# Kernel optimization log

Measured on AMD Instinct MI355X. Metric: run time of the kernel, lower is better.

## Reference

```python
import jax, jax.numpy as jnp
import numpy as np
from jax import lax

B, L, D = 4, 4096, 1024
EXPAND, K = 2, 4
INNER = D * EXPAND  # 2048


def setup_inputs() -> dict:
    key = jax.random.key(0)
    k0, k1, k2, k3, k4 = jax.random.split(key, 5)
    s = 0.02
    return {
        "x": jax.random.normal(k0, (B, L, D), jnp.float32),
        "W_in": jax.random.normal(k1, (D, 2 * INNER), jnp.float32) * s,
        "conv_w": jax.random.normal(k2, (INNER, 1, K), jnp.float32) * s,  # depthwise [out, in/groups=1, k]
        "conv_b": jax.random.normal(k3, (INNER,), jnp.float32) * s,
        "W_out": jax.random.normal(k4, (INNER, D), jnp.float32) * s,
    }


def reference(x, W_in, conv_w, conv_b, W_out):
    # Linear (no bias): [B,L,D] -> [B,L,2*INNER]
    h = jnp.einsum("bld,df->blf", x, W_in)
    # GLU(dim=-1): first half gated by sigmoid of second half
    a, g = jnp.split(h, 2, axis=-1)
    h = a * jax.nn.sigmoid(g)  # [B,L,INNER]
    # depthwise causal Conv1d: torch pads both sides by K-1 then slices [:, :, :L],
    # which equals left-padding by K-1 only.
    hc = jnp.transpose(h, (0, 2, 1))  # [B,INNER,L]
    y = lax.conv_general_dilated(
        hc, conv_w,
        window_strides=(1,),
        padding=[(K - 1, 0)],
        dimension_numbers=("NCH", "OIH", "NCH"),
        feature_group_count=INNER,
    ) + conv_b[None, :, None]  # [B,INNER,L]
    y = jax.nn.silu(y)
    y = jnp.transpose(y, (0, 2, 1))  # [B,L,INNER]
    # Output linear (no bias): [B,L,INNER] -> [B,L,D]
    return jnp.einsum("blf,fd->bld", y, W_out)
```

## Files before the change

kernel.cpp:

```cpp
#include <hip/hip_runtime.h>
#include <hip/hip_bf16.h>

constexpr int B_ = 4, L_ = 4096, D_ = 1024, INNER_ = 2048;
constexpr int M_ = B_ * L_;
constexpr int N1_ = 2 * INNER_;

typedef __attribute__((ext_vector_type(4))) float f32x4;
typedef __attribute__((ext_vector_type(8))) short short8;

#define DEV static __device__ __forceinline__

DEV short f2bfs(float f) {
  __hip_bfloat16 h = __float2bfloat16(f);
  return __builtin_bit_cast(short, h);
}
DEV float bfs2f(short s) {
  unsigned int u = ((unsigned int)(unsigned short)s) << 16;
  return __builtin_bit_cast(float, u);
}

DEV void gload_lds16(const void* g, void* l) {
  __builtin_amdgcn_global_load_lds(
      (const __attribute__((address_space(1))) unsigned int*)g,
      (__attribute__((address_space(3))) unsigned int*)l,
      16, 0, 0);
}

__global__ void k_cvt(const float4* __restrict__ in, short4* __restrict__ out, int n4) {
  int i = blockIdx.x * blockDim.x + threadIdx.x;
  if (i >= n4) return;
  float4 v = in[i];
  short4 o;
  o.x = f2bfs(v.x); o.y = f2bfs(v.y); o.z = f2bfs(v.z); o.w = f2bfs(v.w);
  out[i] = o;
}

__global__ void k_transpose_cvt(const float* __restrict__ W, short* __restrict__ Wt,
                                int R, int C) {
  __shared__ short tile[32][33];
  int tx = threadIdx.x & 31;
  int ty = threadIdx.x >> 5;
  int c0 = blockIdx.x * 32;
  int r0 = blockIdx.y * 32;
#pragma unroll
  for (int i = 0; i < 32; i += 8)
    tile[ty + i][tx] = f2bfs(W[(size_t)(r0 + ty + i) * C + (c0 + tx)]);
  __syncthreads();
#pragma unroll
  for (int i = 0; i < 32; i += 8)
    Wt[(size_t)(c0 + ty + i) * R + (r0 + tx)] = tile[tx][ty + i];
}

__global__ __launch_bounds__(256, 2) void k_gemm1_glu(
    const short* __restrict__ A, const short* __restrict__ Bt,
    short* __restrict__ G) {
  constexpr int K = 1024, BK = 32, NK = K / BK;
  __shared__ short sA[128 * 32];
  __shared__ short sBa[128 * 32];
  __shared__ short sBg[128 * 32];

  const int tid = threadIdx.x;
  const int wid = tid >> 6;
  const int lane = tid & 63;
  const int m0 = blockIdx.x * 128;
  const int n0 = blockIdx.y * 128;

  const int srow = wid * 32 + (lane >> 2);
  const int scol = (lane & 3) * 8;

  const int wr = wid >> 1, wc = wid & 1;
  const int l16 = lane & 15, kg = lane >> 4;

  const f32x4 vzero = {0.f, 0.f, 0.f, 0.f};
  f32x4 acc_a[4][4], acc_g[4][4];
#pragma unroll
  for (int m = 0; m < 4; ++m)
#pragma unroll
    for (int n = 0; n < 4; ++n) { acc_a[m][n] = vzero; acc_g[m][n] = vzero; }

  for (int kt = 0; kt < NK; ++kt) {
    const int k0 = kt * BK;
#pragma unroll
    for (int j = 0; j < 2; ++j) {
      const int r = srow + j * 16;
      gload_lds16(A + (size_t)(m0 + r) * K + k0 + scol, &sA[(wid * 32 + j * 16) * 32]);
      gload_lds16(Bt + (size_t)(n0 + r) * K + k0 + scol, &sBa[(wid * 32 + j * 16) * 32]);
      gload_lds16(Bt + (size_t)(n0 + 2048 + r) * K + k0 + scol, &sBg[(wid * 32 + j * 16) * 32]);
    }
    __syncthreads();

    short8 af[4], ba[4], bg[4];
#pragma unroll
    for (int m = 0; m < 4; ++m)
      af[m] = *(const short8*)&sA[(wr * 64 + m * 16 + l16) * 32 + kg * 8];
#pragma unroll
    for (int n = 0; n < 4; ++n) {
      ba[n] = *(const short8*)&sBa[(wc * 64 + n * 16 + l16) * 32 + kg * 8];
      bg[n] = *(const short8*)&sBg[(wc * 64 + n * 16 + l16) * 32 + kg * 8];
    }
#pragma unroll
    for (int m = 0; m < 4; ++m)
#pragma unroll
      for (int n = 0; n < 4; ++n) {
        acc_a[m][n] = __builtin_amdgcn_mfma_f32_16x16x32_bf16(af[m], ba[n], acc_a[m][n], 0, 0, 0);
        acc_g[m][n] = __builtin_amdgcn_mfma_f32_16x16x32_bf16(af[m], bg[n], acc_g[m][n], 0, 0, 0);
      }
    __syncthreads();
  }

#pragma unroll
  for (int m = 0; m < 4; ++m) {
    const int row0 = m0 + wr * 64 + m * 16 + (lane >> 4) * 4;
#pragma unroll
    for (int n = 0; n < 4; ++n) {
      const int col = n0 + wc * 64 + n * 16 + l16;
#pragma unroll
      for (int r = 0; r < 4; ++r) {
        float a = acc_a[m][n][r];
        float g = acc_g[m][n][r];
        float v = a / (1.f + __expf(-g));
        G[(size_t)(row0 + r) * 2048 + col] = f2bfs(v);
      }
    }
  }
}

__global__ void k_conv_silu(const short* __restrict__ G, const float* __restrict__ w,
                            const float* __restrict__ bias, short* __restrict__ Y) {
  const int t = threadIdx.x;
  const int c0 = t * 8;
  const int b = blockIdx.y;
  const int l0 = blockIdx.x * 16;
  const size_t base = ((size_t)b * L_) * INNER_ + c0;

  float wv[4][8], bv[8];
#pragma unroll
  for (int j = 0; j < 8; ++j) bv[j] = bias[c0 + j];
#pragma unroll
  for (int k = 0; k < 4; ++k)
#pragma unroll
    for (int j = 0; j < 8; ++j) wv[k][j] = w[(c0 + j) * 4 + k];

  float h[3][8];
#pragma unroll
  for (int p = 0; p < 3; ++p) {
    const int l = l0 - 3 + p;
    if (l < 0) {
#pragma unroll
      for (int j = 0; j < 8; ++j) h[p][j] = 0.f;
    } else {
      short8 v = *(const short8*)(G + base + (size_t)l * INNER_);
#pragma unroll
      for (int j = 0; j < 8; ++j) h[p][j] = bfs2f(v[j]);
    }
  }

  for (int i = 0; i < 16; ++i) {
    const int l = l0 + i;
    short8 v = *(const short8*)(G + base + (size_t)l * INNER_);
    short8 o;
#pragma unroll
    for (int j = 0; j < 8; ++j) {
      float g0 = bfs2f(v[j]);
      float y = bv[j] + wv[0][j] * h[0][j] + wv[1][j] * h[1][j] + wv[2][j] * h[2][j] + wv[3][j] * g0;
      y = y / (1.f + __expf(-y));
      o[j] = f2bfs(y);
      h[0][j] = h[1][j]; h[1][j] = h[2][j]; h[2][j] = g0;
    }
    *(short8*)(Y + base + (size_t)l * INNER_) = o;
  }
}

__global__ __launch_bounds__(256, 2) void k_gemm2(
    const short* __restrict__ A, const short* __restrict__ Bt,
    float* __restrict__ Out) {
  constexpr int K = 2048, BK = 32, NK = K / BK;
  __shared__ short sA[128 * 32];
  __shared__ short sB[128 * 32];

  const int tid = threadIdx.x;
  const int wid = tid >> 6;
  const int lane = tid & 63;
  const int m0 = blockIdx.x * 128;
  const int n0 = blockIdx.y * 128;

  const int srow = wid * 32 + (lane >> 2);
  const int scol = (lane & 3) * 8;

  const int wr = wid >> 1, wc = wid & 1;
  const int l16 = lane & 15, kg = lane >> 4;

  const f32x4 vzero = {0.f, 0.f, 0.f, 0.f};
  f32x4 acc[4][4];
#pragma unroll
  for (int m = 0; m < 4; ++m)
#pragma unroll
    for (int n = 0; n < 4; ++n) acc[m][n] = vzero;

  for (int kt = 0; kt < NK; ++kt) {
    const int k0 = kt * BK;
#pragma unroll
    for (int j = 0; j < 2; ++j) {
      const int r = srow + j * 16;
      gload_lds16(A + (size_t)(m0 + r) * K + k0 + scol, &sA[(wid * 32 + j * 16) * 32]);
      gload_lds16(Bt + (size_t)(n0 + r) * K + k0 + scol, &sB[(wid * 32 + j * 16) * 32]);
    }
    __syncthreads();

    short8 af[4], bf[4];
#pragma unroll
    for (int m = 0; m < 4; ++m)
      af[m] = *(const short8*)&sA[(wr * 64 + m * 16 + l16) * 32 + kg * 8];
#pragma unroll
    for (int n = 0; n < 4; ++n)
      bf[n] = *(const short8*)&sB[(wc * 64 + n * 16 + l16) * 32 + kg * 8];
#pragma unroll
    for (int m = 0; m < 4; ++m)
#pragma unroll
      for (int n = 0; n < 4; ++n)
        acc[m][n] = __builtin_amdgcn_mfma_f32_16x16x32_bf16(af[m], bf[n], acc[m][n], 0, 0, 0);
    __syncthreads();
  }

#pragma unroll
  for (int m = 0; m < 4; ++m) {
    const int row0 = m0 + wr * 64 + m * 16 + (lane >> 4) * 4;
#pragma unroll
    for (int n = 0; n < 4; ++n) {
      const int col = n0 + wc * 64 + n * 16 + l16;
#pragma unroll
      for (int r = 0; r < 4; ++r)
        Out[(size_t)(row0 + r) * 1024 + col] = acc[m][n][r];
    }
  }
}

extern "C" void kernel_launch(void* const* d_in, const int* in_sizes, int n_in,
                              void* d_out, int out_size, void* d_ws, size_t ws_size,
                              hipStream_t stream) {
  (void)in_sizes; (void)n_in; (void)out_size; (void)ws_size;
  const float* x      = (const float*)d_in[0];
  const float* W_in   = (const float*)d_in[1];
  const float* conv_w = (const float*)d_in[2];
  const float* conv_b = (const float*)d_in[3];
  const float* W_out  = (const float*)d_in[4];
  float* out = (float*)d_out;

  char* ws = (char*)d_ws;
  size_t off = 0;
  auto alloc = [&](size_t bytes) {
    char* p = ws + off;
    off += (bytes + 255) & ~(size_t)255;
    return p;
  };
  short* Xb    = (short*)alloc((size_t)M_ * D_ * 2);
  short* WinT  = (short*)alloc((size_t)N1_ * D_ * 2);
  short* WoutT = (short*)alloc((size_t)D_ * INNER_ * 2);
  short* G     = (short*)alloc((size_t)M_ * INNER_ * 2);
  short* Y     = (short*)alloc((size_t)M_ * INNER_ * 2);

  k_cvt<<<(M_ * D_ / 4 + 255) / 256, 256, 0, stream>>>(
      (const float4*)x, (short4*)Xb, M_ * D_ / 4);
  k_transpose_cvt<<<dim3(N1_ / 32, D_ / 32), 256, 0, stream>>>(W_in, WinT, D_, N1_);
  k_transpose_cvt<<<dim3(D_ / 32, INNER_ / 32), 256, 0, stream>>>(W_out, WoutT, INNER_, D_);

  k_gemm1_glu<<<dim3(M_ / 128, INNER_ / 128), 256, 0, stream>>>(Xb, WinT, G);
  k_conv_silu<<<dim3(L_ / 16, B_), 256, 0, stream>>>(G, conv_w, conv_b, Y);
  k_gemm2<<<dim3(M_ / 128, D_ / 128), 256, 0, stream>>>(Y, WoutT, out);
}
```

Measured before the change: 396.3 us.

## Replace both GEMMs with a 256x256 multi-stage LDS-pipelined templated kernel

Both GEMMs now run through one templated kernel with 512 threads and 256x256 output tiles. It uses a 4-slot LDS ring filled by direct global-to-LDS loads three stages ahead, with XOR-swizzled LDS addressing to cut bank conflicts. Block indices are swizzled for L2 locality, and s_setprio raises priority around the MFMA bursts. The goal is to hide global memory latency and raise arithmetic intensity over the earlier single-buffered 128x128 kernels. It depends on 128KB of dynamic LDS and hand-placed waitcnt and barrier counts, so correctness rests on exact vmcnt accounting.

```diff
diff --git a/kernel.cpp b/kernel.cpp
--- a/kernel.cpp
+++ b/kernel.cpp
@@ -25,6 +25,10 @@
       (__attribute__((address_space(3))) unsigned int*)l,
       16, 0, 0);
 }
+
+constexpr int VMW8 = 0x0F78;
+constexpr int VMW4 = 0x0F74;
+constexpr int VMW0 = 0x0F70;
 
 __global__ void k_cvt(const float4* __restrict__ in, short4* __restrict__ out, int n4) {
   int i = blockIdx.x * blockDim.x + threadIdx.x;
@@ -51,75 +55,154 @@
     Wt[(size_t)(c0 + ty + i) * R + (r0 + tx)] = tile[tx][ty + i];
 }
 
-__global__ __launch_bounds__(256, 2) void k_gemm1_glu(
+template<int K, bool GLU>
+__global__ __launch_bounds__(512, 2) void k_gemm_pipe(
     const short* __restrict__ A, const short* __restrict__ Bt,
-    short* __restrict__ G) {
-  constexpr int K = 1024, BK = 32, NK = K / BK;
-  __shared__ short sA[128 * 32];
-  __shared__ short sBa[128 * 32];
-  __shared__ short sBg[128 * 32];
-
+    short* __restrict__ OutBf, float* __restrict__ OutF) {
+  extern __shared__ char lds[];
+  constexpr int NT = K / 32;
   const int tid = threadIdx.x;
-  const int wid = tid >> 6;
-  const int lane = tid & 63;
-  const int m0 = blockIdx.x * 128;
-  const int n0 = blockIdx.y * 128;
-
-  const int srow = wid * 32 + (lane >> 2);
-  const int scol = (lane & 3) * 8;
-
+  const int wid = tid >> 6, lane = tid & 63;
+  const int l16 = lane & 15, kg = lane >> 4;
   const int wr = wid >> 1, wc = wid & 1;
-  const int l16 = lane & 15, kg = lane >> 4;
-
-  const f32x4 vzero = {0.f, 0.f, 0.f, 0.f};
-  f32x4 acc_a[4][4], acc_g[4][4];
+
+  const int nwg = (int)gridDim.x;
+  const int bid = (int)blockIdx.x;
+  const int swz = (bid & 7) * (nwg >> 3) + (bid >> 3);
+  const int bm = swz & 63;
+  const int bn = swz >> 6;
+  const int m0 = bm * 256;
+
+  const short* pA[2];
+  const short* pB[2];
+  int ldsA[2], ldsB[2];
+#pragma unroll
+  for (int h = 0; h < 2; ++h) {
+    int p = h * 512 + wid * 64 + lane;
+    int q = p ^ ((p >> 3) & 7);
+    int row = q >> 2, c = q & 3;
+    pA[h] = A + (size_t)(m0 + row) * K + c * 8;
+    int gb;
+    if constexpr (GLU) {
+      gb = bn * 128 + ((row >> 7) << 6) + (row & 63) + (((row >> 6) & 1) ? 2048 : 0);
+    } else {
+      gb = bn * 256 + row;
+    }
+    pB[h] = Bt + (size_t)gb * K + c * 8;
+    ldsA[h] = h * 8192 + wid * 1024;
+    ldsB[h] = 16384 + h * 8192 + wid * 1024;
+  }
+
+  int offA[4], offB[8];
+#pragma unroll
+  for (int m = 0; m < 4; ++m) {
+    int row = wr * 64 + m * 16 + l16;
+    int ch = row * 4 + kg;
+    offA[m] = (ch ^ ((ch >> 3) & 7)) * 16;
+  }
+#pragma unroll
+  for (int n = 0; n < 8; ++n) {
+    int row = wc * 128 + n * 16 + l16;
+    int ch = row * 4 + kg;
+    offB[n] = 16384 + (ch ^ ((ch >> 3) & 7)) * 16;
+  }
+
+  const f32x4 z = {0.f, 0.f, 0.f, 0.f};
+  f32x4 acc[4][8];
 #pragma unroll
   for (int m = 0; m < 4; ++m)
 #pragma unroll
-    for (int n = 0; n < 4; ++n) { acc_a[m][n] = vzero; acc_g[m][n] = vzero; }
-
-  for (int kt = 0; kt < NK; ++kt) {
-    const int k0 = kt * BK;
-#pragma unroll
-    for (int j = 0; j < 2; ++j) {
-      const int r = srow + j * 16;
-      gload_lds16(A + (size_t)(m0 + r) * K + k0 + scol, &sA[(wid * 32 + j * 16) * 32]);
-      gload_lds16(Bt + (size_t)(n0 + r) * K + k0 + scol, &sBa[(wid * 32 + j * 16) * 32]);
-      gload_lds16(Bt + (size_t)(n0 + 2048 + r) * K + k0 + scol, &sBg[(wid * 32 + j * 16) * 32]);
-    }
-    __syncthreads();
-
-    short8 af[4], ba[4], bg[4];
+    for (int n = 0; n < 8; ++n) acc[m][n] = z;
+
+#pragma unroll
+  for (int tt = 0; tt < 3; ++tt) {
+    char* ws = lds + tt * 32768;
+#pragma unroll
+    for (int h = 0; h < 2; ++h) {
+      gload_lds16(pA[h] + tt * 32, ws + ldsA[h]);
+      gload_lds16(pB[h] + tt * 32, ws + ldsB[h]);
+    }
+  }
+#pragma unroll
+  for (int h = 0; h < 2; ++h) { pA[h] += 96; pB[h] += 96; }
+
+  auto iter = [&](int t, bool do_stage) {
+    __builtin_amdgcn_s_barrier();
+    char* slot = lds + (t & 3) * 32768;
+    char* wsl  = lds + ((t + 3) & 3) * 32768;
+    short8 af[4], bfr[4];
+#pragma unroll
+    for (int m = 0; m < 4; ++m) af[m] = *(const short8*)(slot + offA[m]);
+#pragma unroll
+    for (int n = 0; n < 4; ++n) bfr[n] = *(const short8*)(slot + offB[n]);
+    if (do_stage) {
+      gload_lds16(pA[0], wsl + ldsA[0]);
+      gload_lds16(pA[1], wsl + ldsA[1]);
+    }
+    __builtin_amdgcn_s_barrier();
+    asm volatile("s_waitcnt lgkmcnt(0)" ::: "memory");
+    __builtin_amdgcn_sched_barrier(0);
+    __builtin_amdgcn_s_setprio(1);
 #pragma unroll
     for (int m = 0; m < 4; ++m)
-      af[m] = *(const short8*)&sA[(wr * 64 + m * 16 + l16) * 32 + kg * 8];
-#pragma unroll
-    for (int n = 0; n < 4; ++n) {
-      ba[n] = *(const short8*)&sBa[(wc * 64 + n * 16 + l16) * 32 + kg * 8];
-      bg[n] = *(const short8*)&sBg[(wc * 64 + n * 16 + l16) * 32 + kg * 8];
-    }
+#pragma unroll
+      for (int n = 0; n < 4; ++n)
+        acc[m][n] = __builtin_amdgcn_mfma_f32_16x16x32_bf16(af[m], bfr[n], acc[m][n], 0, 0, 0);
+    __builtin_amdgcn_s_setprio(0);
+    __builtin_amdgcn_s_barrier();
+#pragma unroll
+    for (int n = 0; n < 4; ++n) bfr[n] = *(const short8*)(slot + offB[4 + n]);
+    if (do_stage) {
+      gload_lds16(pB[0], wsl + ldsB[0]);
+      gload_lds16(pB[1], wsl + ldsB[1]);
+      pA[0] += 32; pA[1] += 32; pB[0] += 32; pB[1] += 32;
+    }
+    __builtin_amdgcn_s_barrier();
+    asm volatile("s_waitcnt lgkmcnt(0)" ::: "memory");
+    __builtin_amdgcn_sched_barrier(0);
+    __builtin_amdgcn_s_setprio(1);
 #pragma unroll
     for (int m = 0; m < 4; ++m)
 #pragma unroll
+      for (int n = 0; n < 4; ++n)
+        acc[m][4 + n] = __builtin_amdgcn_mfma_f32_16x16x32_bf16(af[m], bfr[n], acc[m][4 + n], 0, 0, 0);
+    __builtin_amdgcn_s_setprio(0);
+  };
+
+  for (int t = 0; t < NT - 3; ++t) {
+    __builtin_amdgcn_s_waitcnt(VMW8);
+    iter(t, true);
+  }
+  __builtin_amdgcn_s_waitcnt(VMW8); iter(NT - 3, false);
+  __builtin_amdgcn_s_waitcnt(VMW4); iter(NT - 2, false);
+  __builtin_amdgcn_s_waitcnt(VMW0); iter(NT - 1, false);
+
+  const int r4 = (lane >> 4) * 4;
+  if constexpr (GLU) {
+#pragma unroll
+    for (int m = 0; m < 4; ++m) {
+      const int row = m0 + wr * 64 + m * 16 + r4;
+#pragma unroll
       for (int n = 0; n < 4; ++n) {
-        acc_a[m][n] = __builtin_amdgcn_mfma_f32_16x16x32_bf16(af[m], ba[n], acc_a[m][n], 0, 0, 0);
-        acc_g[m][n] = __builtin_amdgcn_mfma_f32_16x16x32_bf16(af[m], bg[n], acc_g[m][n], 0, 0, 0);
+        const int col = bn * 128 + wc * 64 + n * 16 + l16;
+#pragma unroll
+        for (int r = 0; r < 4; ++r) {
+          float a = acc[m][n][r];
+          float g = acc[m][4 + n][r];
+          OutBf[(size_t)(row + r) * 2048 + col] = f2bfs(a / (1.f + __expf(-g)));
+        }
       }
-    __syncthreads();
-  }
-
-#pragma unroll
-  for (int m = 0; m < 4; ++m) {
-    const int row0 = m0 + wr * 64 + m * 16 + (lane >> 4) * 4;
-#pragma unroll
-    for (int n = 0; n < 4; ++n) {
-      const int col = n0 + wc * 64 + n * 16 + l16;
-#pragma unroll
-      for (int r = 0; r < 4; ++r) {
-        float a = acc_a[m][n][r];
-        float g = acc_g[m][n][r];
-        float v = a / (1.f + __expf(-g));
-        G[(size_t)(row0 + r) * 2048 + col] = f2bfs(v);
+    }
+  } else {
+#pragma unroll
+    for (int m = 0; m < 4; ++m) {
+      const int row = m0 + wr * 64 + m * 16 + r4;
+#pragma unroll
+      for (int n = 0; n < 8; ++n) {
+        const int col = bn * 256 + wc * 128 + n * 16 + l16;
+#pragma unroll
+        for (int r = 0; r < 4; ++r)
+          OutF[(size_t)(row + r) * 1024 + col] = acc[m][n][r];
       }
     }
   }
@@ -168,70 +251,6 @@
       h[0][j] = h[1][j]; h[1][j] = h[2][j]; h[2][j] = g0;
     }
     *(short8*)(Y + base + (size_t)l * INNER_) = o;
-  }
-}
-
-__global__ __launch_bounds__(256, 2) void k_gemm2(
-    const short* __restrict__ A, const short* __restrict__ Bt,
-    float* __restrict__ Out) {
-  constexpr int K = 2048, BK = 32, NK = K / BK;
-  __shared__ short sA[128 * 32];
-  __shared__ short sB[128 * 32];
-
-  const int tid = threadIdx.x;
-  const int wid = tid >> 6;
-  const int lane = tid & 63;
-  const int m0 = blockIdx.x * 128;
-  const int n0 = blockIdx.y * 128;
-
-  const int srow = wid * 32 + (lane >> 2);
-  const int scol = (lane & 3) * 8;
-
-  const int wr = wid >> 1, wc = wid & 1;
-  const int l16 = lane & 15, kg = lane >> 4;
-
-  const f32x4 vzero = {0.f, 0.f, 0.f, 0.f};
-  f32x4 acc[4][4];
-#pragma unroll
-  for (int m = 0; m < 4; ++m)
-#pragma unroll
-    for (int n = 0; n < 4; ++n) acc[m][n] = vzero;
-
-  for (int kt = 0; kt < NK; ++kt) {
-    const int k0 = kt * BK;
-#pragma unroll
-    for (int j = 0; j < 2; ++j) {
-      const int r = srow + j * 16;
-      gload_lds16(A + (size_t)(m0 + r) * K + k0 + scol, &sA[(wid * 32 + j * 16) * 32]);
-      gload_lds16(Bt + (size_t)(n0 + r) * K + k0 + scol, &sB[(wid * 32 + j * 16) * 32]);
-    }
-    __syncthreads();
-
-    short8 af[4], bf[4];
-#pragma unroll
-    for (int m = 0; m < 4; ++m)
-      af[m] = *(const short8*)&sA[(wr * 64 + m * 16 + l16) * 32 + kg * 8];
-#pragma unroll
-    for (int n = 0; n < 4; ++n)
-      bf[n] = *(const short8*)&sB[(wc * 64 + n * 16 + l16) * 32 + kg * 8];
-#pragma unroll
-    for (int m = 0; m < 4; ++m)
-#pragma unroll
-      for (int n = 0; n < 4; ++n)
-        acc[m][n] = __builtin_amdgcn_mfma_f32_16x16x32_bf16(af[m], bf[n], acc[m][n], 0, 0, 0);
-    __syncthreads();
-  }
-
-#pragma unroll
-  for (int m = 0; m < 4; ++m) {
-    const int row0 = m0 + wr * 64 + m * 16 + (lane >> 4) * 4;
-#pragma unroll
-    for (int n = 0; n < 4; ++n) {
-      const int col = n0 + wc * 64 + n * 16 + l16;
-#pragma unroll
-      for (int r = 0; r < 4; ++r)
-        Out[(size_t)(row0 + r) * 1024 + col] = acc[m][n][r];
-    }
   }
 }
 
@@ -259,12 +278,17 @@
   short* G     = (short*)alloc((size_t)M_ * INNER_ * 2);
   short* Y     = (short*)alloc((size_t)M_ * INNER_ * 2);
 
+  hipFuncSetAttribute((const void*)k_gemm_pipe<1024, true>,
+                      hipFuncAttributeMaxDynamicSharedMemorySize, 131072);
+  hipFuncSetAttribute((const void*)k_gemm_pipe<2048, false>,
+                      hipFuncAttributeMaxDynamicSharedMemorySize, 131072);
+
   k_cvt<<<(M_ * D_ / 4 + 255) / 256, 256, 0, stream>>>(
       (const float4*)x, (short4*)Xb, M_ * D_ / 4);
   k_transpose_cvt<<<dim3(N1_ / 32, D_ / 32), 256, 0, stream>>>(W_in, WinT, D_, N1_);
   k_transpose_cvt<<<dim3(D_ / 32, INNER_ / 32), 256, 0, stream>>>(W_out, WoutT, INNER_, D_);
 
-  k_gemm1_glu<<<dim3(M_ / 128, INNER_ / 128), 256, 0, stream>>>(Xb, WinT, G);
+  k_gemm_pipe<1024, true><<<1024, 512, 131072, stream>>>(Xb, WinT, G, nullptr);
   k_conv_silu<<<dim3(L_ / 16, B_), 256, 0, stream>>>(G, conv_w, conv_b, Y);
-  k_gemm2<<<dim3(M_ / 128, D_ / 128), 256, 0, stream>>>(Y, WoutT, out);
-}
+  k_gemm_pipe<2048, false><<<256, 512, 131072, stream>>>(Y, WoutT, nullptr, out);
+}
```

Result: no change. 395.1 us (-0.3%).
